# Kernel optimization log

Hardware: AMD Instinct MI355X
Metric: run time of the kernel (lower is better)

## Reference

```python
import jax, jax.numpy as jnp
import numpy as np

N_NODES = 50000
N_EDGES = 800000
IN_F = 256
OUT_F = 64
HEADS = 4
NEG_SLOPE = 0.2


def setup_inputs() -> dict:
    key = jax.random.key(0)
    ks = jax.random.split(key, 6)
    x = jax.random.normal(ks[0], (N_NODES, IN_F), dtype=jnp.float32)
    edge_index = jax.random.randint(ks[1], (2, N_EDGES), 0, N_NODES, dtype=jnp.int32)
    edge_weight = jax.random.uniform(ks[2], (N_EDGES,), dtype=jnp.float32)
    # Xavier-uniform-ish scale for params
    gain = float(np.sqrt(2.0 / (1.0 + NEG_SLOPE ** 2)))
    w_bound = gain * np.sqrt(6.0 / (IN_F + OUT_F))
    a_bound = gain * np.sqrt(6.0 / (OUT_F + 1))
    W = jax.random.uniform(ks[3], (HEADS, IN_F, OUT_F), minval=-w_bound, maxval=w_bound, dtype=jnp.float32)
    a_src = jax.random.uniform(ks[4], (HEADS, OUT_F, 1), minval=-a_bound, maxval=a_bound, dtype=jnp.float32)
    a_dst = jax.random.uniform(ks[5], (HEADS, OUT_F, 1), minval=-a_bound, maxval=a_bound, dtype=jnp.float32)
    return {"x": x, "edge_index": edge_index, "edge_weight": edge_weight,
            "W": W, "a_src": a_src, "a_dst": a_dst}


def reference(x, edge_index, edge_weight, W, a_src, a_dst):
    num_nodes = x.shape[0]
    # Per-head linear projection: [H, N, out]
    h = jnp.einsum('ni,hio->hno', x, W)
    # Per-node attention logits, [H, N]
    attn_src = jnp.einsum('hno,hod->hn', h, a_src)
    attn_dst = jnp.einsum('hno,hod->hn', h, a_dst)
    src_idx, dst_idx = edge_index[0], edge_index[1]
    # Per-edge scores [H, E]
    e = attn_src[:, src_idx] + attn_dst[:, dst_idx]
    e = jnp.where(e >= 0, e, NEG_SLOPE * e)  # leaky_relu
    e = e * edge_weight[None, :]
    # Global-max-stabilized exp (matches original: single global max)
    e_exp = jnp.exp(e - jnp.max(e))
    # Segment-softmax denominator per dst node, [H, N]
    denom = jax.ops.segment_sum(e_exp.T, dst_idx, num_segments=num_nodes).T
    alpha = e_exp / (denom[:, dst_idx] + 1e-10)  # [H, E]
    # Weighted messages and scatter-add aggregation
    msg = h[:, src_idx] * alpha[..., None]  # [H, E, out]
    out = jax.vmap(lambda m: jax.ops.segment_sum(m, dst_idx, num_segments=num_nodes))(msg)  # [H, N, out]
    # concat=True: [N, H*out]
    return jnp.transpose(out, (1, 0, 2)).reshape(num_nodes, HEADS * OUT_F)
```

## Files before the change

### kernel.cpp

```cpp
#include <hip/hip_runtime.h>

#define N_NODES 50000
#define N_EDGES 800000
#define IN_F 256
#define OUT_F 64
#define HEADS 4
#define HF 256
#define NEG_SLOPE 0.2f

typedef __bf16 bf16x8 __attribute__((ext_vector_type(8)));
typedef float f32x4 __attribute__((ext_vector_type(4)));

__device__ __forceinline__ unsigned encf(float f) {
  unsigned u = __float_as_uint(f);
  return (u & 0x80000000u) ? ~u : (u | 0x80000000u);
}
__device__ __forceinline__ float decf(unsigned k) {
  unsigned u = (k & 0x80000000u) ? (k & 0x7FFFFFFFu) : ~k;
  return __uint_as_float(u);
}
__device__ __forceinline__ unsigned short f2bf(float f) {
  unsigned u = __float_as_uint(f);
  u += 0x7FFFu + ((u >> 16) & 1u);
  return (unsigned short)(u >> 16);
}
__device__ __forceinline__ float bflo(unsigned u) { return __uint_as_float(u << 16); }
__device__ __forceinline__ float bfhi(unsigned u) { return __uint_as_float(u & 0xFFFF0000u); }

__global__ __launch_bounds__(256) void k_pack_w(const float* __restrict__ W,
                                                unsigned short* __restrict__ wb,
                                                int* __restrict__ deg,
                                                unsigned* __restrict__ gmax) {
  int idx = blockIdx.x * 256 + threadIdx.x;
  if (idx < N_NODES) deg[idx] = 0;
  if (idx == 0) *gmax = 0u;
  int j = idx & 7, l = (idx >> 3) & 63, kt = (idx >> 9) & 7;
  int w = (idx >> 12) & 3, hd = (idx >> 14) & 3;
  int k = kt * 32 + (l >> 4) * 8 + j;
  int o = w * 16 + (l & 15);
  wb[idx] = f2bf(W[((size_t)hd * IN_F + k) * OUT_F + o]);
}

__global__ __launch_bounds__(256) void k_pack_x(const float* __restrict__ x,
                                                unsigned short* __restrict__ xb) {
  int tid = blockIdx.x * 256 + threadIdx.x;
  const float* px = x + (size_t)tid * 8;
  float4 v0 = *(const float4*)px;
  float4 v1 = *(const float4*)(px + 4);
  uint4 o;
  o.x = (unsigned)f2bf(v0.x) | ((unsigned)f2bf(v0.y) << 16);
  o.y = (unsigned)f2bf(v0.z) | ((unsigned)f2bf(v0.w) << 16);
  o.z = (unsigned)f2bf(v1.x) | ((unsigned)f2bf(v1.y) << 16);
  o.w = (unsigned)f2bf(v1.z) | ((unsigned)f2bf(v1.w) << 16);
  *(uint4*)(xb + (size_t)tid * 8) = o;
}

__global__ __launch_bounds__(256) void k_gemm(const unsigned short* __restrict__ xb,
                                              const unsigned short* __restrict__ wb,
                                              const float* __restrict__ a_src,
                                              const float* __restrict__ a_dst,
                                              unsigned short* __restrict__ hb,
                                              float* __restrict__ as_out,
                                              float* __restrict__ ad_out) {
  const int t = threadIdx.x;
  const int hd = t >> 6, l = t & 63;
  const int quad = l >> 4, col = l & 15;
  const int blk = blockIdx.x;
  f32x4 acc[4][4];
#pragma unroll
  for (int ms = 0; ms < 4; ms++)
#pragma unroll
    for (int nt = 0; nt < 4; nt++) acc[ms][nt] = (f32x4){0.f, 0.f, 0.f, 0.f};

  const unsigned short* ab[4];
#pragma unroll
  for (int ms = 0; ms < 4; ms++) {
    int mt = blk * 4 + ms;
    if (mt > 3124) mt = 3124;
    ab[ms] = xb + (size_t)(mt * 16 + col) * IN_F + quad * 8;
  }
  const unsigned short* wbase = wb + (size_t)hd * 16384 + l * 8;

  for (int kt = 0; kt < 8; kt++) {
    union { uint4 u; bf16x8 v; } b[4], a[4];
#pragma unroll
    for (int nt = 0; nt < 4; nt++)
      b[nt].u = *(const uint4*)(wbase + (nt * 8 + kt) * 512);
#pragma unroll
    for (int ms = 0; ms < 4; ms++)
      a[ms].u = *(const uint4*)(ab[ms] + kt * 32);
#pragma unroll
    for (int ms = 0; ms < 4; ms++)
#pragma unroll
      for (int nt = 0; nt < 4; nt++)
        acc[ms][nt] = __builtin_amdgcn_mfma_f32_16x16x32_bf16(a[ms].v, b[nt].v, acc[ms][nt], 0, 0, 0);
  }

  float avs[4], avd[4];
#pragma unroll
  for (int nt = 0; nt < 4; nt++) {
    avs[nt] = a_src[hd * OUT_F + nt * 16 + col];
    avd[nt] = a_dst[hd * OUT_F + nt * 16 + col];
  }
#pragma unroll
  for (int ms = 0; ms < 4; ms++) {
    int mbase = blk * 64 + ms * 16 + quad * 4;
#pragma unroll
    for (int r = 0; r < 4; r++) {
      int m = mbase + r;
      float ps = 0.f, pd = 0.f;
#pragma unroll
      for (int nt = 0; nt < 4; nt++) {
        float hv = acc[ms][nt][r];
        if (m < N_NODES)
          hb[(size_t)m * HF + hd * OUT_F + nt * 16 + col] = f2bf(hv);
        ps += hv * avs[nt];
        pd += hv * avd[nt];
      }
#pragma unroll
      for (int off = 8; off > 0; off >>= 1) {
        ps += __shfl_down(ps, off, 16);
        pd += __shfl_down(pd, off, 16);
      }
      if (col == 0 && m < N_NODES) {
        as_out[m * 4 + hd] = ps;
        ad_out[m * 4 + hd] = pd;
      }
    }
  }
}

__global__ __launch_bounds__(256) void k_edge_max(const int* __restrict__ src,
                                                  const int* __restrict__ dst,
                                                  const float* __restrict__ ew,
                                                  const float* __restrict__ as,
                                                  const float* __restrict__ ad,
                                                  unsigned* __restrict__ gmax,
                                                  int* __restrict__ deg) {
  int e = blockIdx.x * 256 + threadIdx.x;
  int s = src[e], d = dst[e];
  float w = ew[e];
  atomicAdd(deg + d, 1);
  float4 a = *(const float4*)(as + (size_t)s * 4);
  float4 b = *(const float4*)(ad + (size_t)d * 4);
  float v0 = a.x + b.x, v1 = a.y + b.y, v2 = a.z + b.z, v3 = a.w + b.w;
  v0 = v0 >= 0.f ? v0 : NEG_SLOPE * v0;
  v1 = v1 >= 0.f ? v1 : NEG_SLOPE * v1;
  v2 = v2 >= 0.f ? v2 : NEG_SLOPE * v2;
  v3 = v3 >= 0.f ? v3 : NEG_SLOPE * v3;
  float m = fmaxf(fmaxf(v0 * w, v1 * w), fmaxf(v2 * w, v3 * w));
#pragma unroll
  for (int off = 32; off > 0; off >>= 1) m = fmaxf(m, __shfl_down(m, off));
  __shared__ float red[4];
  int wave = threadIdx.x >> 6, lane = threadIdx.x & 63;
  if (lane == 0) red[wave] = m;
  __syncthreads();
  if (threadIdx.x == 0) {
    float mm = fmaxf(fmaxf(red[0], red[1]), fmaxf(red[2], red[3]));
    atomicMax(gmax, encf(mm));
  }
}

__global__ __launch_bounds__(256) void k_scan1(const int* __restrict__ deg,
                                               int* __restrict__ excl,
                                               int* __restrict__ bsum) {
  int i = blockIdx.x * 256 + threadIdx.x;
  int orig = (i < N_NODES) ? deg[i] : 0;
  int v = orig;
  int lane = threadIdx.x & 63, wave = threadIdx.x >> 6;
#pragma unroll
  for (int off = 1; off < 64; off <<= 1) {
    int u = __shfl_up(v, off);
    if (lane >= off) v += u;
  }
  __shared__ int wsum[4];
  if (lane == 63) wsum[wave] = v;
  __syncthreads();
  int base = 0;
  for (int w = 0; w < wave; w++) base += wsum[w];
  int incl = v + base;
  if (i < N_NODES) excl[i] = incl - orig;
  if (threadIdx.x == 255) bsum[blockIdx.x] = incl;
}

__global__ __launch_bounds__(256) void k_scan2(int* __restrict__ bsum, int nb) {
  int t = threadIdx.x;
  int orig = (t < nb) ? bsum[t] : 0;
  int v = orig;
  int lane = t & 63, wave = t >> 6;
#pragma unroll
  for (int off = 1; off < 64; off <<= 1) {
    int u = __shfl_up(v, off);
    if (lane >= off) v += u;
  }
  __shared__ int wsum[4];
  if (lane == 63) wsum[wave] = v;
  __syncthreads();
  int base = 0;
  for (int w = 0; w < wave; w++) base += wsum[w];
  if (t < nb) bsum[t] = v + base - orig;
}

__global__ __launch_bounds__(256) void k_scan3(const int* __restrict__ excl,
                                               const int* __restrict__ bsum,
                                               int* __restrict__ row_start,
                                               int* __restrict__ cursor) {
  int i = blockIdx.x * 256 + threadIdx.x;
  if (i < N_NODES) {
    int rs = excl[i] + bsum[blockIdx.x];
    row_start[i] = rs;
    cursor[i] = rs;
  }
}

__global__ __launch_bounds__(256) void k_scatter(const int* __restrict__ src,
                                                 const int* __restrict__ dst,
                                                 const float* __restrict__ ew,
                                                 int* __restrict__ cursor,
                                                 int2* __restrict__ rec) {
  int e = blockIdx.x * 256 + threadIdx.x;
  int s = src[e], d = dst[e];
  float w = ew[e];
  int pos = atomicAdd(cursor + d, 1);
  rec[pos] = make_int2(s, __float_as_int(w));
}

__global__ __launch_bounds__(256) void k_agg(const int* __restrict__ row_start,
                                             const int* __restrict__ deg,
                                             const int2* __restrict__ rec,
                                             const float* __restrict__ as,
                                             const float* __restrict__ ad,
                                             const unsigned* __restrict__ gmax,
                                             const unsigned short* __restrict__ hb,
                                             float* __restrict__ out) {
  __shared__ float sal[4][4][68];
  const int t = threadIdx.x;
  const int wv = t >> 6, lane = t & 63;
  const int half = lane >> 5, li = lane & 31;
  const int hd8 = li >> 3;
  const int d = blockIdx.x * 4 + wv;
  const int rs = row_start[d];
  const int dg = deg[d];
  const float gm = decf(*gmax);
  const float4 adv = *(const float4*)(ad + (size_t)d * 4);
  float ax = 0.f, ay = 0.f, az = 0.f, aw = 0.f;
  float bx = 0.f, by = 0.f, bz = 0.f, bw = 0.f;
  float den = 0.f;

  for (int j0 = 0; j0 < dg; j0 += 64) {
    const int nj = min(64, dg - j0);
    int se = 0;
    float we = 0.f;
    if (lane < nj) {
      int2 r = rec[rs + j0 + lane];
      se = r.x;
      we = __int_as_float(r.y);
    }
    {
      float4 a4 = *(const float4*)(as + (size_t)se * 4);
      float v0 = a4.x + adv.x;
      float v1 = a4.y + adv.y;
      float v2 = a4.z + adv.z;
      float v3 = a4.w + adv.w;
      v0 = v0 >= 0.f ? v0 : NEG_SLOPE * v0;
      v1 = v1 >= 0.f ? v1 : NEG_SLOPE * v1;
      v2 = v2 >= 0.f ? v2 : NEG_SLOPE * v2;
      v3 = v3 >= 0.f ? v3 : NEG_SLOPE * v3;
      bool ok = lane < nj;
      sal[wv][0][lane] = ok ? __expf(v0 * we - gm) : 0.f;
      sal[wv][1][lane] = ok ? __expf(v1 * we - gm) : 0.f;
      sal[wv][2][lane] = ok ? __expf(v2 * we - gm) : 0.f;
      sal[wv][3][lane] = ok ? __expf(v3 * we - gm) : 0.f;
    }
    asm volatile("s_waitcnt lgkmcnt(0)" ::: "memory");
    const float* salh = sal[wv][hd8];

    int j = 0;
    for (; j + 7 < nj; j += 8) {
      int sj0 = __shfl(se, j + half);
      int sj1 = __shfl(se, j + 2 + half);
      int sj2 = __shfl(se, j + 4 + half);
      int sj3 = __shfl(se, j + 6 + half);
      uint4 q0 = *(const uint4*)(hb + (size_t)sj0 * HF + li * 8);
      uint4 q1 = *(const uint4*)(hb + (size_t)sj1 * HF + li * 8);
      uint4 q2 = *(const uint4*)(hb + (size_t)sj2 * HF + li * 8);
      uint4 q3 = *(const uint4*)(hb + (size_t)sj3 * HF + li * 8);
      float a0 = salh[j + half];
      float a1 = salh[j + 2 + half];
      float a2 = salh[j + 4 + half];
      float a3 = salh[j + 6 + half];
      den += (a0 + a1) + (a2 + a3);
      ax += a0 * bflo(q0.x) + a1 * bflo(q1.x) + a2 * bflo(q2.x) + a3 * bflo(q3.x);
      ay += a0 * bfhi(q0.x) + a1 * bfhi(q1.x) + a2 * bfhi(q2.x) + a3 * bfhi(q3.x);
      az += a0 * bflo(q0.y) + a1 * bflo(q1.y) + a2 * bflo(q2.y) + a3 * bflo(q3.y);
      aw += a0 * bfhi(q0.y) + a1 * bfhi(q1.y) + a2 * bfhi(q2.y) + a3 * bfhi(q3.y);
      bx += a0 * bflo(q0.z) + a1 * bflo(q1.z) + a2 * bflo(q2.z) + a3 * bflo(q3.z);
      by += a0 * bfhi(q0.z) + a1 * bfhi(q1.z) + a2 * bfhi(q2.z) + a3 * bfhi(q3.z);
      bz += a0 * bflo(q0.w) + a1 * bflo(q1.w) + a2 * bflo(q2.w) + a3 * bflo(q3.w);
      bw += a0 * bfhi(q0.w) + a1 * bfhi(q1.w) + a2 * bfhi(q2.w) + a3 * bfhi(q3.w);
    }
    for (; j < nj; j += 2) {
      int sj0 = __shfl(se, min(j + half, nj - 1));
      float a0 = (j + half < nj) ? salh[j + half] : 0.f;
      uint4 q0 = *(const uint4*)(hb + (size_t)sj0 * HF + li * 8);
      den += a0;
      ax += a0 * bflo(q0.x);
      ay += a0 * bfhi(q0.x);
      az += a0 * bflo(q0.y);
      aw += a0 * bfhi(q0.y);
      bx += a0 * bflo(q0.z);
      by += a0 * bfhi(q0.z);
      bz += a0 * bflo(q0.w);
      bw += a0 * bfhi(q0.w);
    }
  }

  ax += __shfl_xor(ax, 32); ay += __shfl_xor(ay, 32);
  az += __shfl_xor(az, 32); aw += __shfl_xor(aw, 32);
  bx += __shfl_xor(bx, 32); by += __shfl_xor(by, 32);
  bz += __shfl_xor(bz, 32); bw += __shfl_xor(bw, 32);
  den += __shfl_xor(den, 32);
  float inv = 1.f / (den + 1e-10f);
  float4 r;
  if (half == 0) r = make_float4(ax * inv, ay * inv, az * inv, aw * inv);
  else           r = make_float4(bx * inv, by * inv, bz * inv, bw * inv);
  *(float4*)(out + (size_t)d * HF + li * 8 + half * 4) = r;
}

extern "C" void kernel_launch(void* const* d_in, const int* in_sizes, int n_in,
                              void* d_out, int out_size, void* d_ws, size_t ws_size,
                              hipStream_t stream) {
  const float* x     = (const float*)d_in[0];
  const int*   ei    = (const int*)d_in[1];
  const float* ew    = (const float*)d_in[2];
  const float* W     = (const float*)d_in[3];
  const float* a_src = (const float*)d_in[4];
  const float* a_dst = (const float*)d_in[5];
  float* out = (float*)d_out;

  unsigned short* hb = (unsigned short*)d_ws;
  unsigned short* xb = hb + (size_t)N_NODES * HF;
  unsigned short* wbp = xb + (size_t)N_NODES * IN_F;
  float* as = (float*)(wbp + 65536);
  float* ad = as + (size_t)HEADS * N_NODES;
  int* deg       = (int*)(ad + (size_t)HEADS * N_NODES);
  int* excl      = deg + N_NODES;
  int* row_start = excl + N_NODES;
  int* cursor    = row_start + N_NODES;
  int2* rec      = (int2*)(cursor + N_NODES);
  int* bsum      = (int*)(rec + N_EDGES);
  unsigned* gmax = (unsigned*)(bsum + 256);

  const int* src = ei;
  const int* dst = ei + N_EDGES;
  const int NB = (N_NODES + 255) / 256;

  k_pack_w<<<256, 256, 0, stream>>>(W, wbp, deg, gmax);
  k_pack_x<<<6250, 256, 0, stream>>>(x, xb);
  k_gemm<<<782, 256, 0, stream>>>(xb, wbp, a_src, a_dst, hb, as, ad);
  k_edge_max<<<N_EDGES / 256, 256, 0, stream>>>(src, dst, ew, as, ad, gmax, deg);
  k_scan1<<<NB, 256, 0, stream>>>(deg, excl, bsum);
  k_scan2<<<1, 256, 0, stream>>>(bsum, NB);
  k_scan3<<<NB, 256, 0, stream>>>(excl, bsum, row_start, cursor);
  k_scatter<<<N_EDGES / 256, 256, 0, stream>>>(src, dst, ew, cursor, rec);
  k_agg<<<N_NODES / 4, 256, 0, stream>>>(row_start, deg, rec, as, ad, gmax, hb, out);
}
```

Before: 310.9 us.

## Fuse all GAT stages into one cooperative persistent kernel with grid syncs

Replaces the chain of nine kernel launches (pack, GEMM, edge max, three-stage scan, scatter, aggregation) with a single cooperative kernel that runs each phase in grid-stride loops separated by grid-wide barriers. It is meant to remove launch overhead and inter-kernel gaps, and to shrink the scan to a per-block segment scan plus one block-level pass. The cost is that the grid is capped to resident blocks (at most 1024), so GEMM and edge phases run with fewer blocks. Grid syncs are also expensive. The old multi-kernel path is kept as a fallback if the cooperative launch fails.

```diff
diff --git a/kernel.cpp b/kernel.cpp
--- a/kernel.cpp
+++ b/kernel.cpp
@@ -1,4 +1,7 @@
 #include <hip/hip_runtime.h>
+#include <hip/hip_cooperative_groups.h>
+
+namespace cg = cooperative_groups;
 
 #define N_NODES 50000
 #define N_EDGES 800000
@@ -26,6 +29,309 @@
 }
 __device__ __forceinline__ float bflo(unsigned u) { return __uint_as_float(u << 16); }
 __device__ __forceinline__ float bfhi(unsigned u) { return __uint_as_float(u & 0xFFFF0000u); }
+
+__global__ __launch_bounds__(256, 4) void k_all(
+    const float* __restrict__ x, const int* __restrict__ src,
+    const int* __restrict__ dst, const float* __restrict__ ew,
+    const float* __restrict__ W, const float* __restrict__ a_src,
+    const float* __restrict__ a_dst, unsigned short* __restrict__ xb,
+    unsigned short* __restrict__ wb, unsigned short* __restrict__ hb,
+    float* __restrict__ as, float* __restrict__ ad, int* __restrict__ deg,
+    int* __restrict__ row_start, int* __restrict__ cursor,
+    int2* __restrict__ rec, int* __restrict__ bsum,
+    unsigned* __restrict__ gmax, float* __restrict__ out) {
+  cg::grid_group gg = cg::this_grid();
+  __shared__ float sal[4][4][68];
+  __shared__ float redf[4];
+  __shared__ int redi[4];
+
+  const int t = threadIdx.x;
+  const int nb = gridDim.x;
+  const int nth = nb * 256;
+  const int tid = blockIdx.x * 256 + t;
+  const int wv = t >> 6, lane = t & 63;
+  const int npb = (N_NODES + nb - 1) / nb;
+
+  for (int i = tid; i < 65536; i += nth) {
+    int j = i & 7, l = (i >> 3) & 63, kt = (i >> 9) & 7;
+    int w = (i >> 12) & 3, hd = (i >> 14) & 3;
+    int k = kt * 32 + (l >> 4) * 8 + j;
+    int o = w * 16 + (l & 15);
+    wb[i] = f2bf(W[((size_t)hd * IN_F + k) * OUT_F + o]);
+  }
+  for (int i = tid; i < N_NODES; i += nth) deg[i] = 0;
+  if (tid == 0) *gmax = 0u;
+  for (int i = tid; i < N_NODES * IN_F / 8; i += nth) {
+    const float* px = x + (size_t)i * 8;
+    float4 v0 = *(const float4*)px;
+    float4 v1 = *(const float4*)(px + 4);
+    uint4 o;
+    o.x = (unsigned)f2bf(v0.x) | ((unsigned)f2bf(v0.y) << 16);
+    o.y = (unsigned)f2bf(v0.z) | ((unsigned)f2bf(v0.w) << 16);
+    o.z = (unsigned)f2bf(v1.x) | ((unsigned)f2bf(v1.y) << 16);
+    o.w = (unsigned)f2bf(v1.z) | ((unsigned)f2bf(v1.w) << 16);
+    *(uint4*)(xb + (size_t)i * 8) = o;
+  }
+  __threadfence();
+  gg.sync();
+
+  for (int blk = blockIdx.x; blk < 782; blk += nb) {
+    const int hd = wv, quad = lane >> 4, col = lane & 15;
+    f32x4 acc[4][4];
+#pragma unroll
+    for (int ms = 0; ms < 4; ms++)
+#pragma unroll
+      for (int nt = 0; nt < 4; nt++) acc[ms][nt] = (f32x4){0.f, 0.f, 0.f, 0.f};
+
+    const unsigned short* ab[4];
+#pragma unroll
+    for (int ms = 0; ms < 4; ms++) {
+      int mt = blk * 4 + ms;
+      if (mt > 3124) mt = 3124;
+      ab[ms] = xb + (size_t)(mt * 16 + col) * IN_F + quad * 8;
+    }
+    const unsigned short* wbase = wb + (size_t)hd * 16384 + lane * 8;
+
+    for (int kt = 0; kt < 8; kt++) {
+      union { uint4 u; bf16x8 v; } b[4], a[4];
+#pragma unroll
+      for (int nt = 0; nt < 4; nt++)
+        b[nt].u = *(const uint4*)(wbase + (nt * 8 + kt) * 512);
+#pragma unroll
+      for (int ms = 0; ms < 4; ms++)
+        a[ms].u = *(const uint4*)(ab[ms] + kt * 32);
+#pragma unroll
+      for (int ms = 0; ms < 4; ms++)
+#pragma unroll
+        for (int nt = 0; nt < 4; nt++)
+          acc[ms][nt] = __builtin_amdgcn_mfma_f32_16x16x32_bf16(a[ms].v, b[nt].v, acc[ms][nt], 0, 0, 0);
+    }
+
+    float avs[4], avd[4];
+#pragma unroll
+    for (int nt = 0; nt < 4; nt++) {
+      avs[nt] = a_src[hd * OUT_F + nt * 16 + col];
+      avd[nt] = a_dst[hd * OUT_F + nt * 16 + col];
+    }
+#pragma unroll
+    for (int ms = 0; ms < 4; ms++) {
+      int mbase = blk * 64 + ms * 16 + quad * 4;
+#pragma unroll
+      for (int r = 0; r < 4; r++) {
+        int m = mbase + r;
+        float ps = 0.f, pd = 0.f;
+#pragma unroll
+        for (int nt = 0; nt < 4; nt++) {
+          float hv = acc[ms][nt][r];
+          if (m < N_NODES)
+            hb[(size_t)m * HF + hd * OUT_F + nt * 16 + col] = f2bf(hv);
+          ps += hv * avs[nt];
+          pd += hv * avd[nt];
+        }
+#pragma unroll
+        for (int off = 8; off > 0; off >>= 1) {
+          ps += __shfl_down(ps, off, 16);
+          pd += __shfl_down(pd, off, 16);
+        }
+        if (col == 0 && m < N_NODES) {
+          as[m * 4 + hd] = ps;
+          ad[m * 4 + hd] = pd;
+        }
+      }
+    }
+  }
+  __threadfence();
+  gg.sync();
+
+  {
+    float mx = -3.4e38f;
+    for (int e = tid; e < N_EDGES; e += nth) {
+      int s = src[e], d = dst[e];
+      float w = ew[e];
+      atomicAdd(deg + d, 1);
+      float4 a = *(const float4*)(as + (size_t)s * 4);
+      float4 b = *(const float4*)(ad + (size_t)d * 4);
+      float v0 = a.x + b.x, v1 = a.y + b.y, v2 = a.z + b.z, v3 = a.w + b.w;
+      v0 = v0 >= 0.f ? v0 : NEG_SLOPE * v0;
+      v1 = v1 >= 0.f ? v1 : NEG_SLOPE * v1;
+      v2 = v2 >= 0.f ? v2 : NEG_SLOPE * v2;
+      v3 = v3 >= 0.f ? v3 : NEG_SLOPE * v3;
+      mx = fmaxf(mx, fmaxf(fmaxf(v0 * w, v1 * w), fmaxf(v2 * w, v3 * w)));
+    }
+#pragma unroll
+    for (int off = 32; off > 0; off >>= 1) mx = fmaxf(mx, __shfl_down(mx, off));
+    if (lane == 0) redf[wv] = mx;
+    __syncthreads();
+    if (t == 0) {
+      float mm = fmaxf(fmaxf(redf[0], redf[1]), fmaxf(redf[2], redf[3]));
+      atomicMax(gmax, encf(mm));
+    }
+  }
+  __threadfence();
+  gg.sync();
+
+  if (wv == 0) {
+    int base0 = blockIdx.x * npb;
+    int carry = 0;
+    for (int off = 0; off < npb; off += 64) {
+      int i = off + lane;
+      int node = base0 + i;
+      int orig = (i < npb && node < N_NODES) ? deg[node] : 0;
+      int v = orig;
+#pragma unroll
+      for (int s = 1; s < 64; s <<= 1) {
+        int u = __shfl_up(v, s);
+        if (lane >= s) v += u;
+      }
+      if (i < npb && node < N_NODES) row_start[node] = carry + v - orig;
+      carry += __shfl(v, 63);
+    }
+    if (lane == 0) bsum[blockIdx.x] = carry;
+  }
+  __threadfence();
+  gg.sync();
+
+  if (blockIdx.x == 0) {
+    int carry = 0;
+    for (int base = 0; base < nb; base += 256) {
+      int idx = base + t;
+      int orig = (idx < nb) ? bsum[idx] : 0;
+      int v = orig;
+#pragma unroll
+      for (int s = 1; s < 64; s <<= 1) {
+        int u = __shfl_up(v, s);
+        if (lane >= s) v += u;
+      }
+      if (lane == 63) redi[wv] = v;
+      __syncthreads();
+      int wbase = 0;
+      for (int w2 = 0; w2 < wv; w2++) wbase += redi[w2];
+      int btot = redi[0] + redi[1] + redi[2] + redi[3];
+      if (idx < nb) bsum[idx] = carry + wbase + v - orig;
+      carry += btot;
+      __syncthreads();
+    }
+  }
+  __threadfence();
+  gg.sync();
+
+  {
+    int base0 = blockIdx.x * npb;
+    int bo = bsum[blockIdx.x];
+    for (int i = t; i < npb; i += 256) {
+      int node = base0 + i;
+      if (node < N_NODES) {
+        int rs = row_start[node] + bo;
+        row_start[node] = rs;
+        cursor[node] = rs;
+      }
+    }
+  }
+  __threadfence();
+  gg.sync();
+
+  for (int e = tid; e < N_EDGES; e += nth) {
+    int s = src[e], d = dst[e];
+    float w = ew[e];
+    int pos = atomicAdd(cursor + d, 1);
+    rec[pos] = make_int2(s, __float_as_int(w));
+  }
+  __threadfence();
+  gg.sync();
+
+  {
+    const float gm = decf(*gmax);
+    const int half = lane >> 5, li = lane & 31;
+    const int hd8 = li >> 3;
+    for (int d = blockIdx.x * 4 + wv; d < N_NODES; d += nb * 4) {
+      const int rs = row_start[d];
+      const int dg = deg[d];
+      const float4 adv = *(const float4*)(ad + (size_t)d * 4);
+      float ax = 0.f, ay = 0.f, az = 0.f, aw = 0.f;
+      float bx = 0.f, by = 0.f, bz = 0.f, bw = 0.f;
+      float den = 0.f;
+
+      for (int j0 = 0; j0 < dg; j0 += 64) {
+        const int nj = min(64, dg - j0);
+        int se = 0;
+        float we = 0.f;
+        if (lane < nj) {
+          int2 r = rec[rs + j0 + lane];
+          se = r.x;
+          we = __int_as_float(r.y);
+        }
+        {
+          float4 a4 = *(const float4*)(as + (size_t)se * 4);
+          float v0 = a4.x + adv.x;
+          float v1 = a4.y + adv.y;
+          float v2 = a4.z + adv.z;
+          float v3 = a4.w + adv.w;
+          v0 = v0 >= 0.f ? v0 : NEG_SLOPE * v0;
+          v1 = v1 >= 0.f ? v1 : NEG_SLOPE * v1;
+          v2 = v2 >= 0.f ? v2 : NEG_SLOPE * v2;
+          v3 = v3 >= 0.f ? v3 : NEG_SLOPE * v3;
+          bool ok = lane < nj;
+          sal[wv][0][lane] = ok ? __expf(v0 * we - gm) : 0.f;
+          sal[wv][1][lane] = ok ? __expf(v1 * we - gm) : 0.f;
+          sal[wv][2][lane] = ok ? __expf(v2 * we - gm) : 0.f;
+          sal[wv][3][lane] = ok ? __expf(v3 * we - gm) : 0.f;
+        }
+        asm volatile("s_waitcnt lgkmcnt(0)" ::: "memory");
+        const float* salh = sal[wv][hd8];
+
+        int j = 0;
+        for (; j + 7 < nj; j += 8) {
+          int sj0 = __shfl(se, j + half);
+          int sj1 = __shfl(se, j + 2 + half);
+          int sj2 = __shfl(se, j + 4 + half);
+          int sj3 = __shfl(se, j + 6 + half);
+          uint4 q0 = *(const uint4*)(hb + (size_t)sj0 * HF + li * 8);
+          uint4 q1 = *(const uint4*)(hb + (size_t)sj1 * HF + li * 8);
+          uint4 q2 = *(const uint4*)(hb + (size_t)sj2 * HF + li * 8);
+          uint4 q3 = *(const uint4*)(hb + (size_t)sj3 * HF + li * 8);
+          float a0 = salh[j + half];
+          float a1 = salh[j + 2 + half];
+          float a2 = salh[j + 4 + half];
+          float a3 = salh[j + 6 + half];
+          den += (a0 + a1) + (a2 + a3);
+          ax += a0 * bflo(q0.x) + a1 * bflo(q1.x) + a2 * bflo(q2.x) + a3 * bflo(q3.x);
+          ay += a0 * bfhi(q0.x) + a1 * bfhi(q1.x) + a2 * bfhi(q2.x) + a3 * bfhi(q3.x);
+          az += a0 * bflo(q0.y) + a1 * bflo(q1.y) + a2 * bflo(q2.y) + a3 * bflo(q3.y);
+          aw += a0 * bfhi(q0.y) + a1 * bfhi(q1.y) + a2 * bfhi(q2.y) + a3 * bfhi(q3.y);
+          bx += a0 * bflo(q0.z) + a1 * bflo(q1.z) + a2 * bflo(q2.z) + a3 * bflo(q3.z);
+          by += a0 * bfhi(q0.z) + a1 * bfhi(q1.z) + a2 * bfhi(q2.z) + a3 * bfhi(q3.z);
+          bz += a0 * bflo(q0.w) + a1 * bflo(q1.w) + a2 * bflo(q2.w) + a3 * bflo(q3.w);
+          bw += a0 * bfhi(q0.w) + a1 * bfhi(q1.w) + a2 * bfhi(q2.w) + a3 * bfhi(q3.w);
+        }
+        for (; j < nj; j += 2) {
+          int sj0 = __shfl(se, min(j + half, nj - 1));
+          float a0 = (j + half < nj) ? salh[j + half] : 0.f;
+          uint4 q0 = *(const uint4*)(hb + (size_t)sj0 * HF + li * 8);
+          den += a0;
+          ax += a0 * bflo(q0.x);
+          ay += a0 * bfhi(q0.x);
+          az += a0 * bflo(q0.y);
+          aw += a0 * bfhi(q0.y);
+          bx += a0 * bflo(q0.z);
+          by += a0 * bfhi(q0.z);
+          bz += a0 * bflo(q0.w);
+          bw += a0 * bfhi(q0.w);
+        }
+      }
+
+      ax += __shfl_xor(ax, 32); ay += __shfl_xor(ay, 32);
+      az += __shfl_xor(az, 32); aw += __shfl_xor(aw, 32);
+      bx += __shfl_xor(bx, 32); by += __shfl_xor(by, 32);
+      bz += __shfl_xor(bz, 32); bw += __shfl_xor(bw, 32);
+      den += __shfl_xor(den, 32);
+      float inv = 1.f / (den + 1e-10f);
+      float4 r;
+      if (half == 0) r = make_float4(ax * inv, ay * inv, az * inv, aw * inv);
+      else           r = make_float4(bx * inv, by * inv, bz * inv, bw * inv);
+      *(float4*)(out + (size_t)d * HF + li * 8 + half * 4) = r;
+    }
+  }
+}
 
 __global__ __launch_bounds__(256) void k_pack_w(const float* __restrict__ W,
                                                 unsigned short* __restrict__ wb,
@@ -71,7 +377,6 @@
   for (int ms = 0; ms < 4; ms++)
 #pragma unroll
     for (int nt = 0; nt < 4; nt++) acc[ms][nt] = (f32x4){0.f, 0.f, 0.f, 0.f};
-
   const unsigned short* ab[4];
 #pragma unroll
   for (int ms = 0; ms < 4; ms++) {
@@ -80,7 +385,6 @@
     ab[ms] = xb + (size_t)(mt * 16 + col) * IN_F + quad * 8;
   }
   const unsigned short* wbase = wb + (size_t)hd * 16384 + l * 8;
-
   for (int kt = 0; kt < 8; kt++) {
     union { uint4 u; bf16x8 v; } b[4], a[4];
 #pragma unroll
@@ -95,7 +399,6 @@
       for (int nt = 0; nt < 4; nt++)
         acc[ms][nt] = __builtin_amdgcn_mfma_f32_16x16x32_bf16(a[ms].v, b[nt].v, acc[ms][nt], 0, 0, 0);
   }
-
   float avs[4], avd[4];
 #pragma unroll
   for (int nt = 0; nt < 4; nt++) {
@@ -183,9 +486,9 @@
   if (threadIdx.x == 255) bsum[blockIdx.x] = incl;
 }
 
-__global__ __launch_bounds__(256) void k_scan2(int* __restrict__ bsum, int nb) {
+__global__ __launch_bounds__(256) void k_scan2(int* __restrict__ bsum, int nbk) {
   int t = threadIdx.x;
-  int orig = (t < nb) ? bsum[t] : 0;
+  int orig = (t < nbk) ? bsum[t] : 0;
   int v = orig;
   int lane = t & 63, wave = t >> 6;
 #pragma unroll
@@ -198,7 +501,7 @@
   __syncthreads();
   int base = 0;
   for (int w = 0; w < wave; w++) base += wsum[w];
-  if (t < nb) bsum[t] = v + base - orig;
+  if (t < nbk) bsum[t] = v + base - orig;
 }
 
 __global__ __launch_bounds__(256) void k_scan3(const int* __restrict__ excl,
@@ -349,19 +652,49 @@
   int* cursor    = row_start + N_NODES;
   int2* rec      = (int2*)(cursor + N_NODES);
   int* bsum      = (int*)(rec + N_EDGES);
-  unsigned* gmax = (unsigned*)(bsum + 256);
-
-  const int* src = ei;
-  const int* dst = ei + N_EDGES;
-  const int NB = (N_NODES + 255) / 256;
-
-  k_pack_w<<<256, 256, 0, stream>>>(W, wbp, deg, gmax);
-  k_pack_x<<<6250, 256, 0, stream>>>(x, xb);
-  k_gemm<<<782, 256, 0, stream>>>(xb, wbp, a_src, a_dst, hb, as, ad);
-  k_edge_max<<<N_EDGES / 256, 256, 0, stream>>>(src, dst, ew, as, ad, gmax, deg);
-  k_scan1<<<NB, 256, 0, stream>>>(deg, excl, bsum);
-  k_scan2<<<1, 256, 0, stream>>>(bsum, NB);
-  k_scan3<<<NB, 256, 0, stream>>>(excl, bsum, row_start, cursor);
-  k_scatter<<<N_EDGES / 256, 256, 0, stream>>>(src, dst, ew, cursor, rec);
-  k_agg<<<N_NODES / 4, 256, 0, stream>>>(row_start, deg, rec, as, ad, gmax, hb, out);
-}
+  unsigned* gmax = (unsigned*)(bsum + 2048);
+
+  const int* srcp = ei;
+  const int* dstp = ei + N_EDGES;
+
+  static int coopBlocks = -2;
+  if (coopBlocks == -2) {
+    int perCU = 0;
+    hipError_t e = hipOccupancyMaxActiveBlocksPerMultiprocessor(&perCU, k_all, 256, 0);
+    if (e == hipSuccess && perCU > 0) {
+      int cap = perCU * 256;
+      coopBlocks = cap < 1024 ? cap : 1024;
+    } else {
+      coopBlocks = -1;
+    }
+  }
+
+  bool done = false;
+  if (coopBlocks > 0) {
+    void* args[] = {
+      (void*)&x, (void*)&srcp, (void*)&dstp, (void*)&ew, (void*)&W,
+      (void*)&a_src, (void*)&a_dst, (void*)&xb, (void*)&wbp, (void*)&hb,
+      (void*)&as, (void*)&ad, (void*)&deg, (void*)&row_start, (void*)&cursor,
+      (void*)&rec, (void*)&bsum, (void*)&gmax, (void*)&out};
+    hipError_t err = hipLaunchCooperativeKernel((void*)k_all, dim3(coopBlocks),
+                                                dim3(256), args, 0, stream);
+    if (err == hipSuccess) {
+      done = true;
+    } else {
+      coopBlocks = -1;
+    }
+  }
+
+  if (!done) {
+    const int NB = (N_NODES + 255) / 256;
+    k_pack_w<<<256, 256, 0, stream>>>(W, wbp, deg, gmax);
+    k_pack_x<<<6250, 256, 0, stream>>>(x, xb);
+    k_gemm<<<782, 256, 0, stream>>>(xb, wbp, a_src, a_dst, hb, as, ad);
+    k_edge_max<<<N_EDGES / 256, 256, 0, stream>>>(srcp, dstp, ew, as, ad, gmax, deg);
+    k_scan1<<<NB, 256, 0, stream>>>(deg, excl, bsum);
+    k_scan2<<<1, 256, 0, stream>>>(bsum, NB);
+    k_scan3<<<NB, 256, 0, stream>>>(excl, bsum, row_start, cursor);
+    k_scatter<<<N_EDGES / 256, 256, 0, stream>>>(srcp, dstp, ew, cursor, rec);
+    k_agg<<<N_NODES / 4, 256, 0, stream>>>(row_start, deg, rec, as, ad, gmax, hb, out);
+  }
+}
```

Measured after the change: 1.086 ms. +249.2%, slower.

## Fuse prep kernels, move degree scan into GEMM block, merge scatter with max

Applied to the files above, without the earlier changes.

Merges the x and W bf16 packing and the degree histogram into one prep kernel, with the degree array zeroed by a memset beforehand. The three-kernel prefix scan becomes a single-block serial scan run by an extra block of the GEMM launch, overlapping with the matmul. The edge-max and CSR scatter kernels are merged, and the max uses one atomic per wave instead of a block reduction. This cuts the launch count from nine to four plus a memset and drops one pass over the edge list. The trade-off is that the GEMM kernel now finishes only when a 196-iteration serial scan block does, and gmax sees more atomics.

```diff
diff --git a/kernel.cpp b/kernel.cpp
--- a/kernel.cpp
+++ b/kernel.cpp
@@ -27,32 +27,34 @@
 __device__ __forceinline__ float bflo(unsigned u) { return __uint_as_float(u << 16); }
 __device__ __forceinline__ float bfhi(unsigned u) { return __uint_as_float(u & 0xFFFF0000u); }
 
-__global__ __launch_bounds__(256) void k_pack_w(const float* __restrict__ W,
-                                                unsigned short* __restrict__ wb,
-                                                int* __restrict__ deg,
-                                                unsigned* __restrict__ gmax) {
-  int idx = blockIdx.x * 256 + threadIdx.x;
-  if (idx < N_NODES) deg[idx] = 0;
-  if (idx == 0) *gmax = 0u;
-  int j = idx & 7, l = (idx >> 3) & 63, kt = (idx >> 9) & 7;
-  int w = (idx >> 12) & 3, hd = (idx >> 14) & 3;
-  int k = kt * 32 + (l >> 4) * 8 + j;
-  int o = w * 16 + (l & 15);
-  wb[idx] = f2bf(W[((size_t)hd * IN_F + k) * OUT_F + o]);
-}
-
-__global__ __launch_bounds__(256) void k_pack_x(const float* __restrict__ x,
-                                                unsigned short* __restrict__ xb) {
+__global__ __launch_bounds__(256) void k_prep(const float* __restrict__ x,
+                                              const float* __restrict__ W,
+                                              const int* __restrict__ dst,
+                                              unsigned short* __restrict__ xb,
+                                              unsigned short* __restrict__ wb,
+                                              int* __restrict__ deg,
+                                              unsigned* __restrict__ gmax) {
   int tid = blockIdx.x * 256 + threadIdx.x;
-  const float* px = x + (size_t)tid * 8;
-  float4 v0 = *(const float4*)px;
-  float4 v1 = *(const float4*)(px + 4);
-  uint4 o;
-  o.x = (unsigned)f2bf(v0.x) | ((unsigned)f2bf(v0.y) << 16);
-  o.y = (unsigned)f2bf(v0.z) | ((unsigned)f2bf(v0.w) << 16);
-  o.z = (unsigned)f2bf(v1.x) | ((unsigned)f2bf(v1.y) << 16);
-  o.w = (unsigned)f2bf(v1.z) | ((unsigned)f2bf(v1.w) << 16);
-  *(uint4*)(xb + (size_t)tid * 8) = o;
+  {
+    const float* px = x + (size_t)tid * 8;
+    float4 v0 = *(const float4*)px;
+    float4 v1 = *(const float4*)(px + 4);
+    uint4 o;
+    o.x = (unsigned)f2bf(v0.x) | ((unsigned)f2bf(v0.y) << 16);
+    o.y = (unsigned)f2bf(v0.z) | ((unsigned)f2bf(v0.w) << 16);
+    o.z = (unsigned)f2bf(v1.x) | ((unsigned)f2bf(v1.y) << 16);
+    o.w = (unsigned)f2bf(v1.z) | ((unsigned)f2bf(v1.w) << 16);
+    *(uint4*)(xb + (size_t)tid * 8) = o;
+  }
+  if (tid < N_EDGES) atomicAdd(deg + dst[tid], 1);
+  if (tid < 65536) {
+    int j = tid & 7, l = (tid >> 3) & 63, kt = (tid >> 9) & 7;
+    int w = (tid >> 12) & 3, hd = (tid >> 14) & 3;
+    int k = kt * 32 + (l >> 4) * 8 + j;
+    int o = w * 16 + (l & 15);
+    wb[tid] = f2bf(W[((size_t)hd * IN_F + k) * OUT_F + o]);
+  }
+  if (tid == 0) *gmax = 0u;
 }
 
 __global__ __launch_bounds__(256) void k_gemm(const unsigned short* __restrict__ xb,
@@ -61,11 +63,43 @@
                                               const float* __restrict__ a_dst,
                                               unsigned short* __restrict__ hb,
                                               float* __restrict__ as_out,
-                                              float* __restrict__ ad_out) {
+                                              float* __restrict__ ad_out,
+                                              const int* __restrict__ deg,
+                                              int* __restrict__ row_start,
+                                              int* __restrict__ cursor) {
   const int t = threadIdx.x;
-  const int hd = t >> 6, l = t & 63;
-  const int quad = l >> 4, col = l & 15;
   const int blk = blockIdx.x;
+  const int wv = t >> 6, lane = t & 63;
+
+  if (blk == 782) {
+    __shared__ int wsum[4];
+    int carry = 0;
+    for (int base = 0; base < N_NODES; base += 256) {
+      int i = base + t;
+      int orig = (i < N_NODES) ? deg[i] : 0;
+      int v = orig;
+#pragma unroll
+      for (int s = 1; s < 64; s <<= 1) {
+        int u = __shfl_up(v, s);
+        if (lane >= s) v += u;
+      }
+      if (lane == 63) wsum[wv] = v;
+      __syncthreads();
+      int wb_ = 0;
+      for (int w2 = 0; w2 < wv; w2++) wb_ += wsum[w2];
+      int tot = wsum[0] + wsum[1] + wsum[2] + wsum[3];
+      if (i < N_NODES) {
+        int rs = carry + wb_ + v - orig;
+        row_start[i] = rs;
+        cursor[i] = rs;
+      }
+      carry += tot;
+      __syncthreads();
+    }
+    return;
+  }
+
+  const int hd = wv, quad = lane >> 4, col = lane & 15;
   f32x4 acc[4][4];
 #pragma unroll
   for (int ms = 0; ms < 4; ms++)
@@ -79,7 +113,7 @@
     if (mt > 3124) mt = 3124;
     ab[ms] = xb + (size_t)(mt * 16 + col) * IN_F + quad * 8;
   }
-  const unsigned short* wbase = wb + (size_t)hd * 16384 + l * 8;
+  const unsigned short* wbase = wb + (size_t)hd * 16384 + lane * 8;
 
   for (int kt = 0; kt < 8; kt++) {
     union { uint4 u; bf16x8 v; } b[4], a[4];
@@ -130,17 +164,17 @@
   }
 }
 
-__global__ __launch_bounds__(256) void k_edge_max(const int* __restrict__ src,
-                                                  const int* __restrict__ dst,
-                                                  const float* __restrict__ ew,
-                                                  const float* __restrict__ as,
-                                                  const float* __restrict__ ad,
-                                                  unsigned* __restrict__ gmax,
-                                                  int* __restrict__ deg) {
+__global__ __launch_bounds__(256) void k_scatter_max(const int* __restrict__ src,
+                                                     const int* __restrict__ dst,
+                                                     const float* __restrict__ ew,
+                                                     const float* __restrict__ as,
+                                                     const float* __restrict__ ad,
+                                                     int* __restrict__ cursor,
+                                                     int2* __restrict__ rec,
+                                                     unsigned* __restrict__ gmax) {
   int e = blockIdx.x * 256 + threadIdx.x;
   int s = src[e], d = dst[e];
   float w = ew[e];
-  atomicAdd(deg + d, 1);
   float4 a = *(const float4*)(as + (size_t)s * 4);
   float4 b = *(const float4*)(ad + (size_t)d * 4);
   float v0 = a.x + b.x, v1 = a.y + b.y, v2 = a.z + b.z, v3 = a.w + b.w;
@@ -151,76 +185,7 @@
   float m = fmaxf(fmaxf(v0 * w, v1 * w), fmaxf(v2 * w, v3 * w));
 #pragma unroll
   for (int off = 32; off > 0; off >>= 1) m = fmaxf(m, __shfl_down(m, off));
-  __shared__ float red[4];
-  int wave = threadIdx.x >> 6, lane = threadIdx.x & 63;
-  if (lane == 0) red[wave] = m;
-  __syncthreads();
-  if (threadIdx.x == 0) {
-    float mm = fmaxf(fmaxf(red[0], red[1]), fmaxf(red[2], red[3]));
-    atomicMax(gmax, encf(mm));
-  }
-}
-
-__global__ __launch_bounds__(256) void k_scan1(const int* __restrict__ deg,
-                                               int* __restrict__ excl,
-                                               int* __restrict__ bsum) {
-  int i = blockIdx.x * 256 + threadIdx.x;
-  int orig = (i < N_NODES) ? deg[i] : 0;
-  int v = orig;
-  int lane = threadIdx.x & 63, wave = threadIdx.x >> 6;
-#pragma unroll
-  for (int off = 1; off < 64; off <<= 1) {
-    int u = __shfl_up(v, off);
-    if (lane >= off) v += u;
-  }
-  __shared__ int wsum[4];
-  if (lane == 63) wsum[wave] = v;
-  __syncthreads();
-  int base = 0;
-  for (int w = 0; w < wave; w++) base += wsum[w];
-  int incl = v + base;
-  if (i < N_NODES) excl[i] = incl - orig;
-  if (threadIdx.x == 255) bsum[blockIdx.x] = incl;
-}
-
-__global__ __launch_bounds__(256) void k_scan2(int* __restrict__ bsum, int nb) {
-  int t = threadIdx.x;
-  int orig = (t < nb) ? bsum[t] : 0;
-  int v = orig;
-  int lane = t & 63, wave = t >> 6;
-#pragma unroll
-  for (int off = 1; off < 64; off <<= 1) {
-    int u = __shfl_up(v, off);
-    if (lane >= off) v += u;
-  }
-  __shared__ int wsum[4];
-  if (lane == 63) wsum[wave] = v;
-  __syncthreads();
-  int base = 0;
-  for (int w = 0; w < wave; w++) base += wsum[w];
-  if (t < nb) bsum[t] = v + base - orig;
-}
-
-__global__ __launch_bounds__(256) void k_scan3(const int* __restrict__ excl,
-                                               const int* __restrict__ bsum,
-                                               int* __restrict__ row_start,
-                                               int* __restrict__ cursor) {
-  int i = blockIdx.x * 256 + threadIdx.x;
-  if (i < N_NODES) {
-    int rs = excl[i] + bsum[blockIdx.x];
-    row_start[i] = rs;
-    cursor[i] = rs;
-  }
-}
-
-__global__ __launch_bounds__(256) void k_scatter(const int* __restrict__ src,
-                                                 const int* __restrict__ dst,
-                                                 const float* __restrict__ ew,
-                                                 int* __restrict__ cursor,
-                                                 int2* __restrict__ rec) {
-  int e = blockIdx.x * 256 + threadIdx.x;
-  int s = src[e], d = dst[e];
-  float w = ew[e];
+  if ((threadIdx.x & 63) == 0) atomicMax(gmax, encf(m));
   int pos = atomicAdd(cursor + d, 1);
   rec[pos] = make_int2(s, __float_as_int(w));
 }
@@ -344,24 +309,19 @@
   float* as = (float*)(wbp + 65536);
   float* ad = as + (size_t)HEADS * N_NODES;
   int* deg       = (int*)(ad + (size_t)HEADS * N_NODES);
-  int* excl      = deg + N_NODES;
-  int* row_start = excl + N_NODES;
+  int* row_start = deg + N_NODES;
   int* cursor    = row_start + N_NODES;
   int2* rec      = (int2*)(cursor + N_NODES);
-  int* bsum      = (int*)(rec + N_EDGES);
-  unsigned* gmax = (unsigned*)(bsum + 256);
-
-  const int* src = ei;
-  const int* dst = ei + N_EDGES;
-  const int NB = (N_NODES + 255) / 256;
-
-  k_pack_w<<<256, 256, 0, stream>>>(W, wbp, deg, gmax);
-  k_pack_x<<<6250, 256, 0, stream>>>(x, xb);
-  k_gemm<<<782, 256, 0, stream>>>(xb, wbp, a_src, a_dst, hb, as, ad);
-  k_edge_max<<<N_EDGES / 256, 256, 0, stream>>>(src, dst, ew, as, ad, gmax, deg);
-  k_scan1<<<NB, 256, 0, stream>>>(deg, excl, bsum);
-  k_scan2<<<1, 256, 0, stream>>>(bsum, NB);
-  k_scan3<<<NB, 256, 0, stream>>>(excl, bsum, row_start, cursor);
-  k_scatter<<<N_EDGES / 256, 256, 0, stream>>>(src, dst, ew, cursor, rec);
+  unsigned* gmax = (unsigned*)(rec + N_EDGES);
+
+  const int* srcp = ei;
+  const int* dstp = ei + N_EDGES;
+
+  hipMemsetAsync(deg, 0, (size_t)N_NODES * sizeof(int), stream);
+  k_prep<<<6250, 256, 0, stream>>>(x, W, dstp, xb, wbp, deg, gmax);
+  k_gemm<<<783, 256, 0, stream>>>(xb, wbp, a_src, a_dst, hb, as, ad,
+                                  deg, row_start, cursor);
+  k_scatter_max<<<N_EDGES / 256, 256, 0, stream>>>(srcp, dstp, ew, as, ad,
+                                                   cursor, rec, gmax);
   k_agg<<<N_NODES / 4, 256, 0, stream>>>(row_start, deg, rec, as, ad, gmax, hb, out);
 }
```

Result: slower. 507.4 us (+63.2%).
